# Kernel optimization log

Hardware: AMD Instinct MI355X
Metric: run time of the kernel (lower is better)

## Reference

```python
import jax, jax.numpy as jnp
import numpy as np

B_, F_, NB, H, R = 32, 10, 20, 128, 2


def setup_inputs() -> dict:
    key = jax.random.key(0)
    ks = jax.random.split(key, 9)
    return {
        "hidden_states": jax.random.normal(ks[0], (B_, F_, NB, H), jnp.float32),
        "cell_states": jax.random.normal(ks[1], (B_, F_, NB, H), jnp.float32),
        "global_t_state": jax.random.normal(ks[2], (B_, NB, H), jnp.float32),
        "global_s_state": jax.random.normal(ks[3], (B_, F_, H), jnp.float32),
        "p": jax.random.normal(ks[4], (B_, F_, NB, H), jnp.float32),
        "U": jax.random.normal(ks[5], (R, F_, NB, 5, H, H), jnp.float32) * 0.05,
        "Wt": jax.random.normal(ks[6], (R, F_, NB, 5, H, H), jnp.float32) * 0.05,
        "Ws": jax.random.normal(ks[7], (R, F_, NB, 5, H, H), jnp.float32) * 0.05,
        "bias": jax.random.normal(ks[8], (R, F_, NB, 5, H), jnp.float32),
    }


def _run_step(h_int, top_h, left_h, top_c, left_c, U_r, Wt_r, Ws_r, b_r):
    # h_int: [B,F,NB,H]; top_*: [B,NB,H]; left_*: [B,F,H]
    # U_r/Wt_r/Ws_r: [F,NB,5,H,H]; b_r: [F,NB,5,H]
    def frame_body(carry, xs):
        h_above, c_above = carry  # [B, NB, H] (row above in the grid)
        x_row, lh, lc, U_f, Wt_f, Ws_f, b_f = xs

        def bone_body(c2, xs2):
            h_left, c_left = c2  # [B, H]
            x, ht, ct, U, Wt, Ws, b = xs2  # U/Wt/Ws: [5,H,H], b: [5,H]
            # 5 gates fused: order (i, f_s, f_t, o, c)
            z = (jnp.einsum('bh,ghk->bgk', x, U)
                 + jnp.einsum('bh,ghk->bgk', ht, Wt)
                 + jnp.einsum('bh,ghk->bgk', h_left, Ws)
                 + b)
            i_n = jax.nn.sigmoid(z[:, 0])
            f_s = jax.nn.sigmoid(z[:, 1])
            f_t = jax.nn.sigmoid(z[:, 2])
            o_n = jax.nn.sigmoid(z[:, 3])
            c_n = jnp.tanh(z[:, 4])
            c_new = i_n * c_n + f_s * c_left + f_t * ct
            h_new = o_n * jnp.tanh(c_new)
            return (h_new, c_new), (h_new, c_new)

        xs2 = (x_row.swapaxes(0, 1), h_above.swapaxes(0, 1),
               c_above.swapaxes(0, 1), U_f, Wt_f, Ws_f, b_f)
        _, (h_row, c_row) = jax.lax.scan(bone_body, (lh, lc), xs2)
        h_row = h_row.swapaxes(0, 1)  # [B, NB, H]
        c_row = c_row.swapaxes(0, 1)
        return (h_row, c_row), (h_row, c_row)

    xs = (h_int.swapaxes(0, 1), left_h.swapaxes(0, 1), left_c.swapaxes(0, 1),
          U_r, Wt_r, Ws_r, b_r)
    _, (h_new, c_new) = jax.lax.scan(frame_body, (top_h, top_c), xs)
    return h_new.swapaxes(0, 1), c_new.swapaxes(0, 1)  # [B,F,NB,H]


def reference(hidden_states, cell_states, global_t_state, global_s_state, p,
              U, Wt, Ws, bias):
    # c-boundaries are identical across recurrent steps
    top_c = jnp.mean(cell_states, axis=1)   # [B, NB, H]
    left_c = jnp.mean(cell_states, axis=2)  # [B, F, H]
    h_int = p
    c_int = jnp.zeros_like(p)
    for i in range(U.shape[0]):  # decoder_recurrent_steps (small, fixed)
        if i == 0:
            h_t, h_s = hidden_states, hidden_states
        elif i == 1:
            h_t = jnp.concatenate([global_t_state[:, None], hidden_states], axis=1)
            h_s = hidden_states
        else:
            h_t = hidden_states
            h_s = jnp.concatenate([global_s_state[:, :, None], hidden_states], axis=2)
        top_h = jnp.mean(h_t, axis=1)   # h[:,0,1:,:]
        left_h = jnp.mean(h_s, axis=2)  # h[:,1:,0,:]
        h_int, c_int = _run_step(h_int, top_h, left_h, top_c, left_c,
                                 U[i], Wt[i], Ws[i], bias[i])
    return h_int, c_int
```

## Files before the change

### kernel.cpp

```cpp
#include <hip/hip_runtime.h>
#include <cstdint>
#include <cstddef>

#define BB  32
#define FF  10
#define NBN 20
#define HH  128
#define GG  5
#define BSTR (FF*NBN*HH)
#define FSTR (NBN*HH)
#define XPAD 132
#define NCELLS 400
#define SC_SYS __HIP_MEMORY_SCOPE_SYSTEM

struct StageList { int cnt; int cells[20]; };

__device__ __forceinline__ float sigm(float x) {
  return 1.f / (1.f + __expf(-x));
}
__device__ __forceinline__ float tanh_fast(float x) {
  float e = __expf(-2.f * fabsf(x));
  float t = (1.f - e) / (1.f + e);
  return copysignf(t, x);
}
__device__ __forceinline__ void fma4(float4& a, const float4 w, const float h) {
  a.x = fmaf(w.x, h, a.x); a.y = fmaf(w.y, h, a.y);
  a.z = fmaf(w.z, h, a.z); a.w = fmaf(w.w, h, a.w);
}
__device__ __forceinline__ void add4(float4& a, const float4 b) {
  a.x += b.x; a.y += b.y; a.z += b.z; a.w += b.w;
}

__global__ void precompute_kernel(
    const float* __restrict__ hid, const float* __restrict__ cell,
    const float* __restrict__ gt,
    float* __restrict__ top_c, float* __restrict__ left_c,
    float* __restrict__ top_h0, float* __restrict__ top_h1,
    float* __restrict__ left_h) {
  int idx = blockIdx.x * 256 + threadIdx.x;
  const int NTOP = BB * NBN * HH;
  const int NLEFT = BB * FF * HH;
  if (idx < NTOP) {
    int h = idx & (HH - 1);
    int n = (idx >> 7) % NBN;
    int b = idx / (HH * NBN);
    const float* hp = hid + (size_t)b * BSTR + n * HH + h;
    const float* cp = cell + (size_t)b * BSTR + n * HH + h;
    float sh = 0.f, sc = 0.f;
#pragma unroll
    for (int f = 0; f < FF; ++f) { sh += hp[f * FSTR]; sc += cp[f * FSTR]; }
    top_c[idx]  = sc * (1.f / FF);
    top_h0[idx] = sh * (1.f / FF);
    top_h1[idx] = (sh + gt[idx]) * (1.f / (FF + 1));
  } else if (idx < NTOP + NLEFT) {
    int j = idx - NTOP;
    int h = j & (HH - 1);
    int f = (j >> 7) % FF;
    int b = j / (HH * FF);
    const float* hp = hid + (size_t)b * BSTR + f * FSTR + h;
    const float* cp = cell + (size_t)b * BSTR + f * FSTR + h;
    float sh = 0.f, sc = 0.f;
#pragma unroll
    for (int n = 0; n < NBN; ++n) { sh += hp[n * HH]; sc += cp[n * HH]; }
    left_c[j] = sc * (1.f / NBN);
    left_h[j] = sh * (1.f / NBN);
  }
}

__global__ __launch_bounds__(256, 2)
void stage_fused(const float* __restrict__ p,
                 const float* __restrict__ U,
                 const float* __restrict__ Wt,
                 const float* __restrict__ Ws,
                 const float* __restrict__ bias,
                 const float* __restrict__ top_c,
                 const float* __restrict__ left_c,
                 const float* __restrict__ top_h0,
                 const float* __restrict__ top_h1,
                 const float* __restrict__ left_h,
                 float* __restrict__ h0, float* __restrict__ c0,
                 float* __restrict__ out_h, float* __restrict__ out_c,
                 float* __restrict__ Z,
                 int* __restrict__ zcnt,
                 StageList sl) {
  __shared__ __align__(16) float xt[3 * BB * XPAD];
  __shared__ int s_old;

  const int cellIdx = blockIdx.x / 10;
  const int sub = blockIdx.x % 10;
  const int g = sub >> 1, ch = sub & 1;
  const int packed = sl.cells[cellIdx];
  const int r = (packed >> 16) & 0xff;
  const int f = (packed >> 8) & 0xff;
  const int n = packed & 0xff;
  const int cid = r * 200 + f * NBN + n;
  const int t = threadIdx.x;
  const int cellofs = f * FSTR + n * HH;

  const float* hbase = r ? out_h : h0;
  const float* hp; int hbs;
  if (f > 0) { hp = hbase + cellofs - FSTR; hbs = BSTR; }
  else       { hp = (r ? top_h1 : top_h0) + n * HH; hbs = FSTR; }
  const float* lp; int lbs;
  if (n > 0) { lp = hbase + cellofs - HH; lbs = BSTR; }
  else       { lp = left_h + f * HH; lbs = FF * HH; }
  const float* xp = (r ? h0 : p) + cellofs;

  for (int i = t; i < BB * HH; i += 256) {
    int b = i >> 7, k = i & (HH - 1);
    xt[(0 * BB + b) * XPAD + k] = hp[(size_t)b * hbs + k];
    xt[(1 * BB + b) * XPAD + k] = lp[(size_t)b * lbs + k];
    xt[(2 * BB + b) * XPAD + k] = xp[(size_t)b * BSTR + k];
  }
  __syncthreads();

  const int cg = t & 15, bq = (t >> 4) & 3, kh = t >> 6;
  const int col = ch * 64 + cg * 4;
  const size_t wofs = ((size_t)(r * FF + f) * NBN + n) * ((size_t)GG * HH * HH)
                    + (size_t)g * HH * HH + (size_t)(kh * 32) * HH + col;
  const float* wtp = Wt + wofs;
  const float* wsp = Ws + wofs;
  const float* wup = U + wofs;
  const int ka0 = kh * 32;

  float4 acc[8];
#pragma unroll
  for (int i = 0; i < 8; ++i) acc[i] = make_float4(0.f, 0.f, 0.f, 0.f);

  for (int kk = 0; kk < 32; kk += 4) {
    float4 wT[4], wS[4], wU[4];
#pragma unroll
    for (int j = 0; j < 4; ++j) {
      wT[j] = *(const float4*)(wtp + (size_t)(kk + j) * HH);
      wS[j] = *(const float4*)(wsp + (size_t)(kk + j) * HH);
      wU[j] = *(const float4*)(wup + (size_t)(kk + j) * HH);
    }
    const int ka = ka0 + kk;
#pragma unroll
    for (int i = 0; i < 8; ++i) {
      const int b = bq + 4 * i;
      float4 xT = *(const float4*)&xt[(0 * BB + b) * XPAD + ka];
      float4 xS = *(const float4*)&xt[(1 * BB + b) * XPAD + ka];
      float4 xU = *(const float4*)&xt[(2 * BB + b) * XPAD + ka];
      float4 a = acc[i];
      fma4(a, wT[0], xT.x); fma4(a, wT[1], xT.y); fma4(a, wT[2], xT.z); fma4(a, wT[3], xT.w);
      fma4(a, wS[0], xS.x); fma4(a, wS[1], xS.y); fma4(a, wS[2], xS.z); fma4(a, wS[3], xS.w);
      fma4(a, wU[0], xU.x); fma4(a, wU[1], xU.y); fma4(a, wU[2], xU.z); fma4(a, wU[3], xU.w);
      acc[i] = a;
    }
  }

  __syncthreads();
  const int lane = t & 63;
  if (kh > 0) {
    float* rp = xt + (size_t)((kh - 1) * 64 + lane) * 36;
#pragma unroll
    for (int i = 0; i < 8; ++i) *(float4*)(rp + 4 * i) = acc[i];
  }
  __syncthreads();
  if (kh == 0) {
#pragma unroll
    for (int q = 0; q < 3; ++q) {
      const float* rp = xt + (size_t)(q * 64 + lane) * 36;
#pragma unroll
      for (int i = 0; i < 8; ++i) add4(acc[i], *(const float4*)(rp + 4 * i));
    }
    float4 bv = *(const float4*)(bias + ((size_t)(r * FF + f) * NBN + n) * (GG * HH)
                                      + (size_t)g * HH + col);
    float* zbase = Z + (size_t)(f * NBN + n) * (BB * GG * HH) + (size_t)g * HH + col;
#pragma unroll
    for (int i = 0; i < 8; ++i) {
      add4(acc[i], bv);
      *(float4*)(zbase + (size_t)(bq + 4 * i) * (GG * HH)) = acc[i];
    }
  }
  __syncthreads();

  if (t == 0)
    s_old = __hip_atomic_fetch_add(&zcnt[cid], 1, __ATOMIC_ACQ_REL, SC_SYS);
  __syncthreads();

  if (s_old == 9) {
    const int c = t & (HH - 1), bh = t >> 7;
    float* hout = r ? out_h : h0;
    float* cout = r ? out_c : c0;
    const float* ctp; int ctbs;
    if (f > 0) { ctp = cout + cellofs - FSTR; ctbs = BSTR; }
    else       { ctp = top_c + n * HH; ctbs = FSTR; }
    const float* clp; int clbs;
    if (n > 0) { clp = cout + cellofs - HH; clbs = BSTR; }
    else       { clp = left_c + f * HH; clbs = FF * HH; }

    const float* zp = Z + (size_t)(f * NBN + n) * (BB * GG * HH) + c;
#pragma unroll
    for (int j = 0; j < 16; ++j) {
      const int b = bh * 16 + j;
      const float* zb = zp + (size_t)b * (GG * HH);
      float zi = zb[0], zfs = zb[HH], zft = zb[2 * HH], zo = zb[3 * HH], zc = zb[4 * HH];
      float clv = clp[(size_t)b * clbs + c];
      float ctv = ctp[(size_t)b * ctbs + c];
      float iv = sigm(zi), fsv = sigm(zfs), ftv = sigm(zft), ov = sigm(zo);
      float cn = tanh_fast(zc);
      float cnew = fmaf(iv, cn, fmaf(fsv, clv, ftv * ctv));
      float hnew = ov * tanh_fast(cnew);
      hout[(size_t)b * BSTR + cellofs + c] = hnew;
      cout[(size_t)b * BSTR + cellofs + c] = cnew;
    }
  }
}

extern "C" void kernel_launch(void* const* d_in, const int* in_sizes, int n_in,
                              void* d_out, int out_size, void* d_ws, size_t ws_size,
                              hipStream_t stream) {
  const float* hid  = (const float*)d_in[0];
  const float* cell = (const float*)d_in[1];
  const float* gt   = (const float*)d_in[2];
  const float* p    = (const float*)d_in[4];
  const float* U    = (const float*)d_in[5];
  const float* Wt   = (const float*)d_in[6];
  const float* Ws   = (const float*)d_in[7];
  const float* bias = (const float*)d_in[8];

  float* out_h = (float*)d_out;
  float* out_c = out_h + (size_t)BB * BSTR;

  float* w = (float*)d_ws;
  float* h0     = w; w += (size_t)BB * BSTR;
  float* c0     = w; w += (size_t)BB * BSTR;
  float* top_c  = w; w += (size_t)BB * NBN * HH;
  float* left_c = w; w += (size_t)BB * FF * HH;
  float* top_h0 = w; w += (size_t)BB * NBN * HH;
  float* top_h1 = w; w += (size_t)BB * NBN * HH;
  float* left_h = w; w += (size_t)BB * FF * HH;
  float* Z      = w; w += (size_t)FF * NBN * BB * GG * HH;
  int* zcnt = (int*)w;

  hipMemsetAsync(zcnt, 0, NCELLS * sizeof(int), stream);

  const int pre_threads = BB * NBN * HH + BB * FF * HH;
  hipLaunchKernelGGL(precompute_kernel, dim3((pre_threads + 255) / 256), dim3(256),
                     0, stream, hid, cell, gt, top_c, left_c, top_h0, top_h1, left_h);

  for (int d = 0; d < FF + NBN; ++d) {
    StageList sl; sl.cnt = 0;
    for (int r = 0; r < 2; ++r) {
      int dd = d - r;
      for (int f = 0; f < FF; ++f) {
        int n = dd - f;
        if (n >= 0 && n < NBN) sl.cells[sl.cnt++] = (r << 16) | (f << 8) | n;
      }
    }
    if (sl.cnt == 0) continue;
    hipLaunchKernelGGL(stage_fused, dim3(sl.cnt * 10), dim3(256), 0, stream,
                       p, U, Wt, Ws, bias, top_c, left_c, top_h0, top_h1, left_h,
                       h0, c0, out_h, out_c, Z, zcnt, sl);
  }
}
```

Measured before the change: 855.0 us.

## Hoist step-0 input projection into a parallel pre-kernel and double-buffer weight loads

Step 0's input projection (p times U plus bias) has no recurrent dependency, so it is computed for all cells up front in a separate fully parallel kernel that writes Z. The wavefront stage kernel then only does the two recurrent GEMVs for step 0 and accumulates into Z, which removes a third of the serial-path weight traffic for those cells. The k-loop is also rewritten with explicit double-buffered weight register loads so global loads overlap the FMAs. The cost is an extra launch, a read-modify-write of Z in step 0, and higher register pressure from the doubled weight buffers.

```diff
diff --git a/kernel.cpp b/kernel.cpp
--- a/kernel.cpp
+++ b/kernel.cpp
@@ -67,9 +67,92 @@
   }
 }
 
+__global__ __launch_bounds__(256, 4)
+void z0_kernel(const float* __restrict__ p, const float* __restrict__ U,
+               const float* __restrict__ bias, float* __restrict__ Z) {
+  __shared__ __align__(16) float xs[HH][36];
+  const int cell = blockIdx.x / GG, g = blockIdx.x % GG;
+  const int f = cell / NBN, n = cell % NBN;
+  const int t = threadIdx.x;
+  const int cid = t & 31, bq = t >> 5;
+  const int cellofs = f * FSTR + n * HH;
+
+  for (int i = t; i < BB * HH; i += 256) {
+    int b = i >> 7, k = i & (HH - 1);
+    xs[k][b] = p[(size_t)b * BSTR + cellofs + k];
+  }
+  __syncthreads();
+
+  const float* wu = U + (size_t)cell * (GG * HH * HH) + (size_t)g * HH * HH + cid * 4;
+  float4 bv = *(const float4*)(bias + (size_t)cell * (GG * HH) + g * HH + cid * 4);
+  float4 acc[4];
+#pragma unroll
+  for (int j = 0; j < 4; ++j) acc[j] = bv;
+
+#pragma unroll 4
+  for (int k = 0; k < HH; ++k) {
+    float4 w = *(const float4*)(wu + (size_t)k * HH);
+    float4 x = *(const float4*)&xs[k][bq * 4];
+    fma4(acc[0], w, x.x); fma4(acc[1], w, x.y);
+    fma4(acc[2], w, x.z); fma4(acc[3], w, x.w);
+  }
+
+  float* zp = Z + (size_t)cell * (BB * GG * HH) + (size_t)g * HH + cid * 4;
+#pragma unroll
+  for (int j = 0; j < 4; ++j)
+    *(float4*)(zp + (size_t)(bq * 4 + j) * (GG * HH)) = acc[j];
+}
+
+template <int NM>
+__device__ __forceinline__ void gemv_core(
+    const float* __restrict__ wtp, const float* __restrict__ wsp,
+    const float* __restrict__ wup, const float* xt, int ka0, int bq,
+    float4 (&acc)[8]) {
+  float4 wA[3][4], wB[3][4];
+
+#define LW(W, KK) { \
+    _Pragma("unroll") \
+    for (int j = 0; j < 4; ++j) { \
+      W[0][j] = *(const float4*)(wtp + (size_t)((KK) + j) * HH); \
+      W[1][j] = *(const float4*)(wsp + (size_t)((KK) + j) * HH); \
+      if (NM == 3) W[2][j] = *(const float4*)(wup + (size_t)((KK) + j) * HH); \
+    } }
+
+#define CP(W, KK) { \
+    const int ka = ka0 + (KK); \
+    _Pragma("unroll") \
+    for (int i = 0; i < 8; ++i) { \
+      const int b = bq + 4 * i; \
+      float4 xT = *(const float4*)&xt[(0 * BB + b) * XPAD + ka]; \
+      float4 xS = *(const float4*)&xt[(1 * BB + b) * XPAD + ka]; \
+      float4 a = acc[i]; \
+      fma4(a, W[0][0], xT.x); fma4(a, W[0][1], xT.y); \
+      fma4(a, W[0][2], xT.z); fma4(a, W[0][3], xT.w); \
+      fma4(a, W[1][0], xS.x); fma4(a, W[1][1], xS.y); \
+      fma4(a, W[1][2], xS.z); fma4(a, W[1][3], xS.w); \
+      if (NM == 3) { \
+        float4 xU = *(const float4*)&xt[(2 * BB + b) * XPAD + ka]; \
+        fma4(a, W[2][0], xU.x); fma4(a, W[2][1], xU.y); \
+        fma4(a, W[2][2], xU.z); fma4(a, W[2][3], xU.w); \
+      } \
+      acc[i] = a; \
+    } }
+
+  LW(wA, 0)  LW(wB, 4)
+  CP(wA, 0)  LW(wA, 8)
+  CP(wB, 4)  LW(wB, 12)
+  CP(wA, 8)  LW(wA, 16)
+  CP(wB, 12) LW(wB, 20)
+  CP(wA, 16) LW(wA, 24)
+  CP(wB, 20) LW(wB, 28)
+  CP(wA, 24)
+  CP(wB, 28)
+#undef LW
+#undef CP
+}
+
 __global__ __launch_bounds__(256, 2)
-void stage_fused(const float* __restrict__ p,
-                 const float* __restrict__ U,
+void stage_fused(const float* __restrict__ U,
                  const float* __restrict__ Wt,
                  const float* __restrict__ Ws,
                  const float* __restrict__ bias,
@@ -104,13 +187,12 @@
   const float* lp; int lbs;
   if (n > 0) { lp = hbase + cellofs - HH; lbs = BSTR; }
   else       { lp = left_h + f * HH; lbs = FF * HH; }
-  const float* xp = (r ? h0 : p) + cellofs;
 
   for (int i = t; i < BB * HH; i += 256) {
     int b = i >> 7, k = i & (HH - 1);
     xt[(0 * BB + b) * XPAD + k] = hp[(size_t)b * hbs + k];
     xt[(1 * BB + b) * XPAD + k] = lp[(size_t)b * lbs + k];
-    xt[(2 * BB + b) * XPAD + k] = xp[(size_t)b * BSTR + k];
+    if (r) xt[(2 * BB + b) * XPAD + k] = h0[(size_t)b * BSTR + cellofs + k];
   }
   __syncthreads();
 
@@ -127,28 +209,8 @@
 #pragma unroll
   for (int i = 0; i < 8; ++i) acc[i] = make_float4(0.f, 0.f, 0.f, 0.f);
 
-  for (int kk = 0; kk < 32; kk += 4) {
-    float4 wT[4], wS[4], wU[4];
-#pragma unroll
-    for (int j = 0; j < 4; ++j) {
-      wT[j] = *(const float4*)(wtp + (size_t)(kk + j) * HH);
-      wS[j] = *(const float4*)(wsp + (size_t)(kk + j) * HH);
-      wU[j] = *(const float4*)(wup + (size_t)(kk + j) * HH);
-    }
-    const int ka = ka0 + kk;
-#pragma unroll
-    for (int i = 0; i < 8; ++i) {
-      const int b = bq + 4 * i;
-      float4 xT = *(const float4*)&xt[(0 * BB + b) * XPAD + ka];
-      float4 xS = *(const float4*)&xt[(1 * BB + b) * XPAD + ka];
-      float4 xU = *(const float4*)&xt[(2 * BB + b) * XPAD + ka];
-      float4 a = acc[i];
-      fma4(a, wT[0], xT.x); fma4(a, wT[1], xT.y); fma4(a, wT[2], xT.z); fma4(a, wT[3], xT.w);
-      fma4(a, wS[0], xS.x); fma4(a, wS[1], xS.y); fma4(a, wS[2], xS.z); fma4(a, wS[3], xS.w);
-      fma4(a, wU[0], xU.x); fma4(a, wU[1], xU.y); fma4(a, wU[2], xU.z); fma4(a, wU[3], xU.w);
-      acc[i] = a;
-    }
-  }
+  if (r) gemv_core<3>(wtp, wsp, wup, xt, ka0, bq, acc);
+  else   gemv_core<2>(wtp, wsp, wup, xt, ka0, bq, acc);
 
   __syncthreads();
   const int lane = t & 63;
@@ -165,13 +227,20 @@
 #pragma unroll
       for (int i = 0; i < 8; ++i) add4(acc[i], *(const float4*)(rp + 4 * i));
     }
-    float4 bv = *(const float4*)(bias + ((size_t)(r * FF + f) * NBN + n) * (GG * HH)
-                                      + (size_t)g * HH + col);
     float* zbase = Z + (size_t)(f * NBN + n) * (BB * GG * HH) + (size_t)g * HH + col;
-#pragma unroll
-    for (int i = 0; i < 8; ++i) {
-      add4(acc[i], bv);
-      *(float4*)(zbase + (size_t)(bq + 4 * i) * (GG * HH)) = acc[i];
+    if (r) {
+      float4 bv = *(const float4*)(bias + (((size_t)(FF + f) * NBN + n) * GG + g) * HH + col);
+#pragma unroll
+      for (int i = 0; i < 8; ++i) {
+        add4(acc[i], bv);
+        *(float4*)(zbase + (size_t)(bq + 4 * i) * (GG * HH)) = acc[i];
+      }
+    } else {
+#pragma unroll
+      for (int i = 0; i < 8; ++i) {
+        float4* dst = (float4*)(zbase + (size_t)(bq + 4 * i) * (GG * HH));
+        float4 o = *dst; add4(o, acc[i]); *dst = o;
+      }
     }
   }
   __syncthreads();
@@ -241,6 +310,9 @@
   hipLaunchKernelGGL(precompute_kernel, dim3((pre_threads + 255) / 256), dim3(256),
                      0, stream, hid, cell, gt, top_c, left_c, top_h0, top_h1, left_h);
 
+  hipLaunchKernelGGL(z0_kernel, dim3(FF * NBN * GG), dim3(256), 0, stream,
+                     p, U, bias, Z);
+
   for (int d = 0; d < FF + NBN; ++d) {
     StageList sl; sl.cnt = 0;
     for (int r = 0; r < 2; ++r) {
@@ -252,7 +324,7 @@
     }
     if (sl.cnt == 0) continue;
     hipLaunchKernelGGL(stage_fused, dim3(sl.cnt * 10), dim3(256), 0, stream,
-                       p, U, Wt, Ws, bias, top_c, left_c, top_h0, top_h1, left_h,
+                       U, Wt, Ws, bias, top_c, left_c, top_h0, top_h1, left_h,
                        h0, c0, out_h, out_c, Z, zcnt, sl);
   }
 }
```

Measured after the change: 951.1 us. +11.2%, slower.

## Convert weights to bf16 and precompute first-step input projection outside wavefront

Applied to the files above, without the earlier changes.

A new kernel converts U, Wt and Ws to bf16 on every call, roughly halving the weight bytes streamed by the wavefront stage kernels. Another new kernel computes the step-0 input projection U·p plus bias for all cells before the diagonal sweep. That takes one of the three GEMV terms off the critical path for r=0 cells, which then accumulate into the precomputed Z. Stage blocks grow to 512 threads with fewer batch rows per thread. The cost is an extra full pass over the fp32 weights, reduced weight precision, and a read-modify-write of Z.

```diff
diff --git a/kernel.cpp b/kernel.cpp
--- a/kernel.cpp
+++ b/kernel.cpp
@@ -11,6 +11,7 @@
 #define FSTR (NBN*HH)
 #define XPAD 132
 #define NCELLS 400
+#define WELEM 32768000
 #define SC_SYS __HIP_MEMORY_SCOPE_SYSTEM
 
 struct StageList { int cnt; int cells[20]; };
@@ -29,6 +30,39 @@
 }
 __device__ __forceinline__ void add4(float4& a, const float4 b) {
   a.x += b.x; a.y += b.y; a.z += b.z; a.w += b.w;
+}
+__device__ __forceinline__ float4 ldw(const unsigned short* p) {
+  uint2 u = *(const uint2*)p;
+  float4 r;
+  r.x = __uint_as_float(u.x << 16);
+  r.y = __uint_as_float(u.x & 0xffff0000u);
+  r.z = __uint_as_float(u.y << 16);
+  r.w = __uint_as_float(u.y & 0xffff0000u);
+  return r;
+}
+__device__ __forceinline__ unsigned int bf16_rtn(float f) {
+  unsigned int u = __float_as_uint(f);
+  return (u + 0x7FFFu + ((u >> 16) & 1u)) >> 16;
+}
+
+__global__ __launch_bounds__(256)
+void convert_kernel(const float* __restrict__ U, const float* __restrict__ Wt,
+                    const float* __restrict__ Ws,
+                    unsigned short* __restrict__ Ub, unsigned short* __restrict__ Wtb,
+                    unsigned short* __restrict__ Wsb) {
+  const int per = WELEM / 2048;
+  const int a = blockIdx.x / per, bo = blockIdx.x % per;
+  const float* src = (a == 0) ? U : (a == 1) ? Wt : Ws;
+  unsigned short* dst = (a == 0) ? Ub : (a == 1) ? Wtb : Wsb;
+  const size_t base = ((size_t)bo * 256 + threadIdx.x) * 8;
+  float4 v0 = *(const float4*)(src + base);
+  float4 v1 = *(const float4*)(src + base + 4);
+  uint4 o;
+  o.x = bf16_rtn(v0.x) | (bf16_rtn(v0.y) << 16);
+  o.y = bf16_rtn(v0.z) | (bf16_rtn(v0.w) << 16);
+  o.z = bf16_rtn(v1.x) | (bf16_rtn(v1.y) << 16);
+  o.w = bf16_rtn(v1.z) | (bf16_rtn(v1.w) << 16);
+  *(uint4*)(dst + base) = o;
 }
 
 __global__ void precompute_kernel(
@@ -67,11 +101,78 @@
   }
 }
 
-__global__ __launch_bounds__(256, 2)
-void stage_fused(const float* __restrict__ p,
-                 const float* __restrict__ U,
-                 const float* __restrict__ Wt,
-                 const float* __restrict__ Ws,
+__global__ __launch_bounds__(256, 4)
+void z0_kernel(const float* __restrict__ p, const unsigned short* __restrict__ Ub,
+               const float* __restrict__ bias, float* __restrict__ Z) {
+  __shared__ __align__(16) float xs[HH][36];
+  const int cell = blockIdx.x / GG, g = blockIdx.x % GG;
+  const int f = cell / NBN, n = cell % NBN;
+  const int t = threadIdx.x;
+  const int cid = t & 31, bq = t >> 5;
+  const int cellofs = f * FSTR + n * HH;
+
+  for (int i = t; i < BB * HH; i += 256) {
+    int b = i >> 7, k = i & (HH - 1);
+    xs[k][b] = p[(size_t)b * BSTR + cellofs + k];
+  }
+  __syncthreads();
+
+  const unsigned short* wu = Ub + (size_t)cell * (GG * HH * HH)
+                           + (size_t)g * HH * HH + cid * 4;
+  float4 bv = *(const float4*)(bias + (size_t)cell * (GG * HH) + g * HH + cid * 4);
+  float4 acc[4];
+#pragma unroll
+  for (int j = 0; j < 4; ++j) acc[j] = bv;
+
+#pragma unroll 4
+  for (int k = 0; k < HH; ++k) {
+    float4 w = ldw(wu + (size_t)k * HH);
+    float4 x = *(const float4*)&xs[k][bq * 4];
+    fma4(acc[0], w, x.x); fma4(acc[1], w, x.y);
+    fma4(acc[2], w, x.z); fma4(acc[3], w, x.w);
+  }
+
+  float* zp = Z + (size_t)cell * (BB * GG * HH) + (size_t)g * HH + cid * 4;
+#pragma unroll
+  for (int j = 0; j < 4; ++j)
+    *(float4*)(zp + (size_t)(bq * 4 + j) * (GG * HH)) = acc[j];
+}
+
+template <int NM>
+__device__ __forceinline__ void gemv_core(
+    const unsigned short* __restrict__ wtp, const unsigned short* __restrict__ wsp,
+    const unsigned short* __restrict__ wup, const float* xt, int ka0, int bq,
+    float4 (&acc)[4]) {
+  for (int kk = 0; kk < 32; kk += 4) {
+    float4 wT[4], wS[4], wU[4];
+#pragma unroll
+    for (int j = 0; j < 4; ++j) {
+      wT[j] = ldw(wtp + (size_t)(kk + j) * HH);
+      wS[j] = ldw(wsp + (size_t)(kk + j) * HH);
+      if (NM == 3) wU[j] = ldw(wup + (size_t)(kk + j) * HH);
+    }
+    const int ka = ka0 + kk;
+#pragma unroll
+    for (int i = 0; i < 4; ++i) {
+      const int b = bq + 8 * i;
+      float4 xT = *(const float4*)&xt[(0 * BB + b) * XPAD + ka];
+      float4 xS = *(const float4*)&xt[(1 * BB + b) * XPAD + ka];
+      float4 a = acc[i];
+      fma4(a, wT[0], xT.x); fma4(a, wT[1], xT.y); fma4(a, wT[2], xT.z); fma4(a, wT[3], xT.w);
+      fma4(a, wS[0], xS.x); fma4(a, wS[1], xS.y); fma4(a, wS[2], xS.z); fma4(a, wS[3], xS.w);
+      if (NM == 3) {
+        float4 xU = *(const float4*)&xt[(2 * BB + b) * XPAD + ka];
+        fma4(a, wU[0], xU.x); fma4(a, wU[1], xU.y); fma4(a, wU[2], xU.z); fma4(a, wU[3], xU.w);
+      }
+      acc[i] = a;
+    }
+  }
+}
+
+__global__ __launch_bounds__(512, 2)
+void stage_fused(const unsigned short* __restrict__ Ub,
+                 const unsigned short* __restrict__ Wtb,
+                 const unsigned short* __restrict__ Wsb,
                  const float* __restrict__ bias,
                  const float* __restrict__ top_c,
                  const float* __restrict__ left_c,
@@ -104,74 +205,60 @@
   const float* lp; int lbs;
   if (n > 0) { lp = hbase + cellofs - HH; lbs = BSTR; }
   else       { lp = left_h + f * HH; lbs = FF * HH; }
-  const float* xp = (r ? h0 : p) + cellofs;
-
-  for (int i = t; i < BB * HH; i += 256) {
+
+  for (int i = t; i < BB * HH; i += 512) {
     int b = i >> 7, k = i & (HH - 1);
     xt[(0 * BB + b) * XPAD + k] = hp[(size_t)b * hbs + k];
     xt[(1 * BB + b) * XPAD + k] = lp[(size_t)b * lbs + k];
-    xt[(2 * BB + b) * XPAD + k] = xp[(size_t)b * BSTR + k];
-  }
-  __syncthreads();
-
-  const int cg = t & 15, bq = (t >> 4) & 3, kh = t >> 6;
+    if (r) xt[(2 * BB + b) * XPAD + k] = h0[(size_t)b * BSTR + cellofs + k];
+  }
+  __syncthreads();
+
+  const int cg = t & 15, bq = (t >> 4) & 7, kh = t >> 7;
   const int col = ch * 64 + cg * 4;
   const size_t wofs = ((size_t)(r * FF + f) * NBN + n) * ((size_t)GG * HH * HH)
                     + (size_t)g * HH * HH + (size_t)(kh * 32) * HH + col;
-  const float* wtp = Wt + wofs;
-  const float* wsp = Ws + wofs;
-  const float* wup = U + wofs;
+  const unsigned short* wtp = Wtb + wofs;
+  const unsigned short* wsp = Wsb + wofs;
+  const unsigned short* wup = Ub + wofs;
   const int ka0 = kh * 32;
 
-  float4 acc[8];
-#pragma unroll
-  for (int i = 0; i < 8; ++i) acc[i] = make_float4(0.f, 0.f, 0.f, 0.f);
-
-  for (int kk = 0; kk < 32; kk += 4) {
-    float4 wT[4], wS[4], wU[4];
-#pragma unroll
-    for (int j = 0; j < 4; ++j) {
-      wT[j] = *(const float4*)(wtp + (size_t)(kk + j) * HH);
-      wS[j] = *(const float4*)(wsp + (size_t)(kk + j) * HH);
-      wU[j] = *(const float4*)(wup + (size_t)(kk + j) * HH);
-    }
-    const int ka = ka0 + kk;
-#pragma unroll
-    for (int i = 0; i < 8; ++i) {
-      const int b = bq + 4 * i;
-      float4 xT = *(const float4*)&xt[(0 * BB + b) * XPAD + ka];
-      float4 xS = *(const float4*)&xt[(1 * BB + b) * XPAD + ka];
-      float4 xU = *(const float4*)&xt[(2 * BB + b) * XPAD + ka];
-      float4 a = acc[i];
-      fma4(a, wT[0], xT.x); fma4(a, wT[1], xT.y); fma4(a, wT[2], xT.z); fma4(a, wT[3], xT.w);
-      fma4(a, wS[0], xS.x); fma4(a, wS[1], xS.y); fma4(a, wS[2], xS.z); fma4(a, wS[3], xS.w);
-      fma4(a, wU[0], xU.x); fma4(a, wU[1], xU.y); fma4(a, wU[2], xU.z); fma4(a, wU[3], xU.w);
-      acc[i] = a;
-    }
-  }
-
-  __syncthreads();
-  const int lane = t & 63;
+  float4 acc[4];
+#pragma unroll
+  for (int i = 0; i < 4; ++i) acc[i] = make_float4(0.f, 0.f, 0.f, 0.f);
+
+  if (r) gemv_core<3>(wtp, wsp, wup, xt, ka0, bq, acc);
+  else   gemv_core<2>(wtp, wsp, wup, xt, ka0, bq, acc);
+
+  __syncthreads();
+  const int pair = bq * 16 + cg;
   if (kh > 0) {
-    float* rp = xt + (size_t)((kh - 1) * 64 + lane) * 36;
-#pragma unroll
-    for (int i = 0; i < 8; ++i) *(float4*)(rp + 4 * i) = acc[i];
+    float* rp = xt + (size_t)((kh - 1) * 128 + pair) * 20;
+#pragma unroll
+    for (int i = 0; i < 4; ++i) *(float4*)(rp + 4 * i) = acc[i];
   }
   __syncthreads();
   if (kh == 0) {
 #pragma unroll
     for (int q = 0; q < 3; ++q) {
-      const float* rp = xt + (size_t)(q * 64 + lane) * 36;
-#pragma unroll
-      for (int i = 0; i < 8; ++i) add4(acc[i], *(const float4*)(rp + 4 * i));
-    }
-    float4 bv = *(const float4*)(bias + ((size_t)(r * FF + f) * NBN + n) * (GG * HH)
-                                      + (size_t)g * HH + col);
+      const float* rp = xt + (size_t)(q * 128 + pair) * 20;
+#pragma unroll
+      for (int i = 0; i < 4; ++i) add4(acc[i], *(const float4*)(rp + 4 * i));
+    }
     float* zbase = Z + (size_t)(f * NBN + n) * (BB * GG * HH) + (size_t)g * HH + col;
-#pragma unroll
-    for (int i = 0; i < 8; ++i) {
-      add4(acc[i], bv);
-      *(float4*)(zbase + (size_t)(bq + 4 * i) * (GG * HH)) = acc[i];
+    if (r) {
+      float4 bv = *(const float4*)(bias + (((size_t)(FF + f) * NBN + n) * GG + g) * HH + col);
+#pragma unroll
+      for (int i = 0; i < 4; ++i) {
+        add4(acc[i], bv);
+        *(float4*)(zbase + (size_t)(bq + 8 * i) * (GG * HH)) = acc[i];
+      }
+    } else {
+#pragma unroll
+      for (int i = 0; i < 4; ++i) {
+        float4* dst = (float4*)(zbase + (size_t)(bq + 8 * i) * (GG * HH));
+        float4 o = *dst; add4(o, acc[i]); *dst = o;
+      }
     }
   }
   __syncthreads();
@@ -193,8 +280,8 @@
 
     const float* zp = Z + (size_t)(f * NBN + n) * (BB * GG * HH) + c;
 #pragma unroll
-    for (int j = 0; j < 16; ++j) {
-      const int b = bh * 16 + j;
+    for (int j = 0; j < 8; ++j) {
+      const int b = bh * 8 + j;
       const float* zb = zp + (size_t)b * (GG * HH);
       float zi = zb[0], zfs = zb[HH], zft = zb[2 * HH], zo = zb[3 * HH], zc = zb[4 * HH];
       float clv = clp[(size_t)b * clbs + c];
@@ -233,13 +320,22 @@
   float* top_h1 = w; w += (size_t)BB * NBN * HH;
   float* left_h = w; w += (size_t)BB * FF * HH;
   float* Z      = w; w += (size_t)FF * NBN * BB * GG * HH;
-  int* zcnt = (int*)w;
+  int* zcnt = (int*)w; w += 512;
+  unsigned short* Ub  = (unsigned short*)w;
+  unsigned short* Wtb = Ub + (size_t)WELEM;
+  unsigned short* Wsb = Wtb + (size_t)WELEM;
 
   hipMemsetAsync(zcnt, 0, NCELLS * sizeof(int), stream);
+
+  hipLaunchKernelGGL(convert_kernel, dim3(3 * (WELEM / 2048)), dim3(256), 0, stream,
+                     U, Wt, Ws, Ub, Wtb, Wsb);
 
   const int pre_threads = BB * NBN * HH + BB * FF * HH;
   hipLaunchKernelGGL(precompute_kernel, dim3((pre_threads + 255) / 256), dim3(256),
                      0, stream, hid, cell, gt, top_c, left_c, top_h0, top_h1, left_h);
+
+  hipLaunchKernelGGL(z0_kernel, dim3(FF * NBN * GG), dim3(256), 0, stream,
+                     p, Ub, bias, Z);
 
   for (int d = 0; d < FF + NBN; ++d) {
     StageList sl; sl.cnt = 0;
@@ -251,8 +347,8 @@
       }
     }
     if (sl.cnt == 0) continue;
-    hipLaunchKernelGGL(stage_fused, dim3(sl.cnt * 10), dim3(256), 0, stream,
-                       p, U, Wt, Ws, bias, top_c, left_c, top_h0, top_h1, left_h,
+    hipLaunchKernelGGL(stage_fused, dim3(sl.cnt * 10), dim3(512), 0, stream,
+                       Ub, Wtb, Wsb, bias, top_c, left_c, top_h0, top_h1, left_h,
                        h0, c0, out_h, out_c, Z, zcnt, sl);
   }
 }
```

After: 839.7 us. Within noise of the previous version (-1.8%).
